# Optimization experiments

Measured on AMD Instinct MI355X. Metric: run time of the kernel, lower is better.

## Reference

```python
import jax, jax.numpy as jnp
import numpy as np

NUM_EMBEDDINGS = 1024
EMBEDDING_DIM = 64


def setup_inputs() -> dict:
    key = jax.random.key(0)
    kx, kc = jax.random.split(key)
    x = jax.random.normal(kx, (32, 64, 64, EMBEDDING_DIM), dtype=jnp.float32)
    # flax nn.Embed default init: normal(stddev=1.0)
    codebook = jax.random.normal(kc, (NUM_EMBEDDINGS, EMBEDDING_DIM), dtype=jnp.float32)
    return {"x": x, "codebook": codebook}


def reference(x, codebook):
    # x: [B, H, W, D] -> [N, D]
    x_flat = x.reshape(-1, EMBEDDING_DIM)
    distances = (
        jnp.sum(x_flat ** 2, axis=1, keepdims=True)
        - 2.0 * jnp.dot(x_flat, codebook.T)
        + jnp.sum(codebook ** 2, axis=1)
    )
    idx = jnp.argmin(distances, axis=1)                      # [N]
    discrete = jax.nn.one_hot(idx, NUM_EMBEDDINGS, dtype=x.dtype)  # [N, K]
    quantized = jnp.dot(discrete, codebook)                  # [N, D]
    quantized = quantized.reshape(x.shape[:-1] + (-1,))
    return (discrete, quantized)
```

## Files before the change

kernel.cpp:

```cpp
#include <hip/hip_runtime.h>

#define KCW 1024
#define DIM 64
#define ROWS_BLK 256
#define STRIPE 128
#define CWTILE 128

typedef __attribute__((ext_vector_type(4))) float f32x4;

__global__ void __launch_bounds__(256) vq_cnorm_kernel(const float* __restrict__ cb,
                                                       float* __restrict__ cnorm) {
    int k = blockIdx.x * blockDim.x + threadIdx.x;
    if (k < KCW) {
        const float4* c4 = (const float4*)(cb + (size_t)k * DIM);
        float s0 = 0.f, s1 = 0.f, s2 = 0.f, s3 = 0.f;
#pragma unroll
        for (int j = 0; j < DIM / 4; j += 4) {
            float4 a = c4[j + 0];
            float4 b = c4[j + 1];
            float4 c = c4[j + 2];
            float4 d = c4[j + 3];
            s0 += a.x * a.x + a.y * a.y + a.z * a.z + a.w * a.w;
            s1 += b.x * b.x + b.y * b.y + b.z * b.z + b.w * b.w;
            s2 += c.x * c.x + c.y * c.y + c.z * c.z + c.w * c.w;
            s3 += d.x * d.x + d.y * d.y + d.z * d.z + d.w * d.w;
        }
        cnorm[k] = (s0 + s1) + (s2 + s3);
    }
}

#define DOT4ACC(acc, av, bv)                                               \
    acc = fmaf((av).w, (bv).w,                                             \
          fmaf((av).z, (bv).z,                                             \
          fmaf((av).y, (bv).y,                                             \
          fmaf((av).x, (bv).x, (acc)))));

#define ROWF(P, n)                                                         \
    DOT4ACC(q##n##a.x, r##P##n, c##P##0) DOT4ACC(q##n##a.y, r##P##n, c##P##1) \
    DOT4ACC(q##n##a.z, r##P##n, c##P##2) DOT4ACC(q##n##a.w, r##P##n, c##P##3) \
    DOT4ACC(q##n##b.x, r##P##n, c##P##4) DOT4ACC(q##n##b.y, r##P##n, c##P##5) \
    DOT4ACC(q##n##b.z, r##P##n, c##P##6) DOT4ACC(q##n##b.w, r##P##n, c##P##7)

#define FMAB(P) ROWF(P, 0) ROWF(P, 1) ROWF(P, 2) ROWF(P, 3)                \
                ROWF(P, 4) ROWF(P, 5) ROWF(P, 6) ROWF(P, 7)

#define LOADOPS(P, k4v)                                                    \
    {   const int ka_ = (k4v) ^ ty2;                                       \
        const int kb_ = (k4v) ^ tx2;                                       \
        r##P##0 = sX[abase + ka_ + 0 * 128];                               \
        r##P##1 = sX[abase + ka_ + 1 * 128];                               \
        r##P##2 = sX[abase + ka_ + 2 * 128];                               \
        r##P##3 = sX[abase + ka_ + 3 * 128];                               \
        r##P##4 = sX[abase + ka_ + 4 * 128];                               \
        r##P##5 = sX[abase + ka_ + 5 * 128];                               \
        r##P##6 = sX[abase + ka_ + 6 * 128];                               \
        r##P##7 = sX[abase + ka_ + 7 * 128];                               \
        c##P##0 = sC[bbase + kb_ + 0 * 128];                               \
        c##P##1 = sC[bbase + kb_ + 1 * 128];                               \
        c##P##2 = sC[bbase + kb_ + 2 * 128];                               \
        c##P##3 = sC[bbase + kb_ + 3 * 128];                               \
        c##P##4 = sC[bbase + kb_ + 4 * 128];                               \
        c##P##5 = sC[bbase + kb_ + 5 * 128];                               \
        c##P##6 = sC[bbase + kb_ + 6 * 128];                               \
        c##P##7 = sC[bbase + kb_ + 7 * 128]; }

#define UPROW(n, X)                                                        \
    { float s_ = fmaf(-2.f, q##n##X, cn);                                  \
      if (s_ < best##n) { best##n = s_; bidx##n = cwv; } }

#define UPCOL(c, X)                                                        \
    { const float cn = sCn[cnb + 8 * (c)];                                 \
      const int cwv = cwbase + 8 * (c);                                    \
      UPROW(0, X) UPROW(1, X) UPROW(2, X) UPROW(3, X)                      \
      UPROW(4, X) UPROW(5, X) UPROW(6, X) UPROW(7, X) }

#define MERGEPUT(n)                                                        \
    { int rl = 64 * wr + ty + 8 * (n);                                     \
      sMs[rl * 16 + slot] = best##n; sMi[rl * 16 + slot] = bidx##n; }

__global__ void __launch_bounds__(256, 2) vq_main_kernel(const float* __restrict__ x,
                                                         const float* __restrict__ cb,
                                                         const float* __restrict__ cnorm,
                                                         float* __restrict__ out_discrete,
                                                         float* __restrict__ out_quant) {
    __shared__ float4 sX[STRIPE * 16];
    __shared__ float4 sC[CWTILE * 16];
    __shared__ float sCn[CWTILE];
    __shared__ int sFinal[STRIPE];

    float* sMs = (float*)sX;
    int* sMi = ((int*)sX) + STRIPE * 16;

    const int tid = threadIdx.x;
    const int wave = tid >> 6;
    const int lane = tid & 63;
    const int wr = wave >> 1;
    const int wc = wave & 1;
    const int ty = lane >> 3;
    const int tx = lane & 7;

    const int row0 = blockIdx.x * ROWS_BLK;
    const float4* xg = (const float4*)x;
    const float4* cbg = (const float4*)cb;
    float4* od4 = (float4*)out_discrete;
    float4* oq4 = (float4*)out_quant;

    const int cnb = 64 * wc + tx;
    const int abase = (64 * wr + ty) * 16;
    const int bbase = (64 * wc + tx) * 16;
    const int ty2 = ty << 1;
    const int tx2 = tx << 1;
    const int slot = wc * 8 + tx;

    for (int s = 0; s < ROWS_BLK / STRIPE; ++s) {
        const int grow0 = row0 + s * STRIPE;

        __syncthreads();

#pragma unroll
        for (int i = 0; i < 8; ++i) {
            int e = i * 256 + tid;
            int r = e >> 4, ch = e & 15;
            sX[r * 16 + (ch ^ ((r & 7) << 1))] = xg[(size_t)(grow0 + r) * 16 + ch];
        }

        float best0 = 3.4e38f, best1 = 3.4e38f, best2 = 3.4e38f, best3 = 3.4e38f;
        float best4 = 3.4e38f, best5 = 3.4e38f, best6 = 3.4e38f, best7 = 3.4e38f;
        int bidx0 = 0, bidx1 = 0, bidx2 = 0, bidx3 = 0;
        int bidx4 = 0, bidx5 = 0, bidx6 = 0, bidx7 = 0;

        for (int p = 0; p < KCW / CWTILE; ++p) {
            __syncthreads();

#pragma unroll
            for (int i = 0; i < 8; ++i) {
                int e = i * 256 + tid;
                int c = e >> 4, ch = e & 15;
                sC[c * 16 + (ch ^ ((c & 7) << 1))] =
                    cbg[(size_t)(p * CWTILE + c) * 16 + ch];
            }
            if (tid < CWTILE) sCn[tid] = cnorm[p * CWTILE + tid];
            __syncthreads();

            float4 q0a = {0.f, 0.f, 0.f, 0.f}, q0b = {0.f, 0.f, 0.f, 0.f};
            float4 q1a = {0.f, 0.f, 0.f, 0.f}, q1b = {0.f, 0.f, 0.f, 0.f};
            float4 q2a = {0.f, 0.f, 0.f, 0.f}, q2b = {0.f, 0.f, 0.f, 0.f};
            float4 q3a = {0.f, 0.f, 0.f, 0.f}, q3b = {0.f, 0.f, 0.f, 0.f};
            float4 q4a = {0.f, 0.f, 0.f, 0.f}, q4b = {0.f, 0.f, 0.f, 0.f};
            float4 q5a = {0.f, 0.f, 0.f, 0.f}, q5b = {0.f, 0.f, 0.f, 0.f};
            float4 q6a = {0.f, 0.f, 0.f, 0.f}, q6b = {0.f, 0.f, 0.f, 0.f};
            float4 q7a = {0.f, 0.f, 0.f, 0.f}, q7b = {0.f, 0.f, 0.f, 0.f};

            float4 rA0, rA1, rA2, rA3, rA4, rA5, rA6, rA7;
            float4 cA0, cA1, cA2, cA3, cA4, cA5, cA6, cA7;
            float4 rB0, rB1, rB2, rB3, rB4, rB5, rB6, rB7;
            float4 cB0, cB1, cB2, cB3, cB4, cB5, cB6, cB7;

            LOADOPS(A, 0)
#pragma unroll
            for (int k4 = 0; k4 < 16; k4 += 2) {
                LOADOPS(B, k4 + 1)
                FMAB(A)
                if (k4 + 2 < 16) LOADOPS(A, k4 + 2)
                FMAB(B)
            }

            const int cwbase = p * CWTILE + 64 * wc + tx;
            UPCOL(0, a.x) UPCOL(1, a.y) UPCOL(2, a.z) UPCOL(3, a.w)
            UPCOL(4, b.x) UPCOL(5, b.y) UPCOL(6, b.z) UPCOL(7, b.w)
        }

        __syncthreads();

        MERGEPUT(0) MERGEPUT(1) MERGEPUT(2) MERGEPUT(3)
        MERGEPUT(4) MERGEPUT(5) MERGEPUT(6) MERGEPUT(7)
        __syncthreads();

        if (tid < STRIPE) {
            float bs = sMs[tid * 16];
            int bi = sMi[tid * 16];
#pragma unroll
            for (int j = 1; j < 16; ++j) {
                float sj = sMs[tid * 16 + j];
                int ij = sMi[tid * 16 + j];
                if (sj < bs || (sj == bs && ij < bi)) { bs = sj; bi = ij; }
            }
            sFinal[tid] = bi;
        }
        __syncthreads();

        {
            size_t obase = (size_t)grow0 * (KCW / 4);
            const int col = tid * 4;
            for (int it = 0; it < STRIPE; ++it) {
                int idx = sFinal[it];
                f32x4 v;
                v.x = (col + 0 == idx) ? 1.f : 0.f;
                v.y = (col + 1 == idx) ? 1.f : 0.f;
                v.z = (col + 2 == idx) ? 1.f : 0.f;
                v.w = (col + 3 == idx) ? 1.f : 0.f;
                __builtin_nontemporal_store(v, (f32x4*)&od4[obase + (size_t)it * 256 + tid]);
            }
            size_t qbase = (size_t)grow0 * 16;
#pragma unroll
            for (int it = 0; it < 8; ++it) {
                int cnk = it * 256 + tid;
                int r = cnk >> 4;
                int ch = cnk & 15;
                float4 qv = cbg[(size_t)sFinal[r] * 16 + ch];
                __builtin_nontemporal_store(*(f32x4*)&qv, (f32x4*)&oq4[qbase + cnk]);
            }
        }
    }
}

extern "C" void kernel_launch(void* const* d_in, const int* in_sizes, int n_in,
                              void* d_out, int out_size, void* d_ws, size_t ws_size,
                              hipStream_t stream) {
    const float* x = (const float*)d_in[0];
    const float* cb = (const float*)d_in[1];
    float* cnorm = (float*)d_ws;

    const int n = in_sizes[0];
    const int rows = n / DIM;

    float* out_discrete = (float*)d_out;
    float* out_quant = (float*)d_out + (size_t)rows * KCW;

    vq_cnorm_kernel<<<(KCW + 255) / 256, 256, 0, stream>>>(cb, cnorm);
    vq_main_kernel<<<rows / ROWS_BLK, 256, 0, stream>>>(x, cb, cnorm, out_discrete, out_quant);
}
```

Before: 816.6 us.

## Keep X stripe rows in registers and split codeword tile into halves

Each thread now preloads its 8 input rows (all 64 dims) from shared memory into a register array once per stripe. The dot-product loop then reads only codebook vectors from shared memory, processing the 8 per-thread codewords in two halves of 4 to cut accumulator count. The aim is to remove the repeated LDS reads of X for every codebook tile. The cost is a 512-float register array per thread, which likely exceeds the VGPR budget under the two-blocks-per-CU launch bound and risks heavy scratch spilling.

```diff
diff --git a/kernel.cpp b/kernel.cpp
--- a/kernel.cpp
+++ b/kernel.cpp
@@ -35,44 +35,34 @@
           fmaf((av).y, (bv).y,                                             \
           fmaf((av).x, (bv).x, (acc)))));
 
-#define ROWF(P, n)                                                         \
-    DOT4ACC(q##n##a.x, r##P##n, c##P##0) DOT4ACC(q##n##a.y, r##P##n, c##P##1) \
-    DOT4ACC(q##n##a.z, r##P##n, c##P##2) DOT4ACC(q##n##a.w, r##P##n, c##P##3) \
-    DOT4ACC(q##n##b.x, r##P##n, c##P##4) DOT4ACC(q##n##b.y, r##P##n, c##P##5) \
-    DOT4ACC(q##n##b.z, r##P##n, c##P##6) DOT4ACC(q##n##b.w, r##P##n, c##P##7)
-
-#define FMAB(P) ROWF(P, 0) ROWF(P, 1) ROWF(P, 2) ROWF(P, 3)                \
-                ROWF(P, 4) ROWF(P, 5) ROWF(P, 6) ROWF(P, 7)
-
-#define LOADOPS(P, k4v)                                                    \
-    {   const int ka_ = (k4v) ^ ty2;                                       \
-        const int kb_ = (k4v) ^ tx2;                                       \
-        r##P##0 = sX[abase + ka_ + 0 * 128];                               \
-        r##P##1 = sX[abase + ka_ + 1 * 128];                               \
-        r##P##2 = sX[abase + ka_ + 2 * 128];                               \
-        r##P##3 = sX[abase + ka_ + 3 * 128];                               \
-        r##P##4 = sX[abase + ka_ + 4 * 128];                               \
-        r##P##5 = sX[abase + ka_ + 5 * 128];                               \
-        r##P##6 = sX[abase + ka_ + 6 * 128];                               \
-        r##P##7 = sX[abase + ka_ + 7 * 128];                               \
-        c##P##0 = sC[bbase + kb_ + 0 * 128];                               \
-        c##P##1 = sC[bbase + kb_ + 1 * 128];                               \
-        c##P##2 = sC[bbase + kb_ + 2 * 128];                               \
-        c##P##3 = sC[bbase + kb_ + 3 * 128];                               \
-        c##P##4 = sC[bbase + kb_ + 4 * 128];                               \
-        c##P##5 = sC[bbase + kb_ + 5 * 128];                               \
-        c##P##6 = sC[bbase + kb_ + 6 * 128];                               \
-        c##P##7 = sC[bbase + kb_ + 7 * 128]; }
-
-#define UPROW(n, X)                                                        \
-    { float s_ = fmaf(-2.f, q##n##X, cn);                                  \
-      if (s_ < best##n) { best##n = s_; bidx##n = cwv; } }
-
-#define UPCOL(c, X)                                                        \
-    { const float cn = sCn[cnb + 8 * (c)];                                 \
-      const int cwv = cwbase + 8 * (c);                                    \
-      UPROW(0, X) UPROW(1, X) UPROW(2, X) UPROW(3, X)                      \
-      UPROW(4, X) UPROW(5, X) UPROW(6, X) UPROW(7, X) }
+#define LOADQ(P, k4v, h)                                                   \
+    {   const int kb_ = ((k4v) ^ tx2);                                     \
+        P##0 = sC[bbase + kb_ + ((h) * 4 + 0) * 128];                      \
+        P##1 = sC[bbase + kb_ + ((h) * 4 + 1) * 128];                      \
+        P##2 = sC[bbase + kb_ + ((h) * 4 + 2) * 128];                      \
+        P##3 = sC[bbase + kb_ + ((h) * 4 + 3) * 128]; }
+
+#define ROWQ(P, n, k4v)                                                    \
+    DOT4ACC(q##n.x, areg[n][(k4v)], P##0)                                  \
+    DOT4ACC(q##n.y, areg[n][(k4v)], P##1)                                  \
+    DOT4ACC(q##n.z, areg[n][(k4v)], P##2)                                  \
+    DOT4ACC(q##n.w, areg[n][(k4v)], P##3)
+
+#define FMAQ(P, k4v) ROWQ(P, 0, (k4v)) ROWQ(P, 1, (k4v)) ROWQ(P, 2, (k4v)) \
+                     ROWQ(P, 3, (k4v)) ROWQ(P, 4, (k4v)) ROWQ(P, 5, (k4v)) \
+                     ROWQ(P, 6, (k4v)) ROWQ(P, 7, (k4v))
+
+#define UPR(n, comp)                                                       \
+    { float s_ = fmaf(-2.f, q##n.comp, cn_);                               \
+      if (s_ < best##n) { best##n = s_; bidx##n = cwv_; } }
+
+#define UPC(c, comp, h)                                                    \
+    { const float cn_ = sCn[cnb + 8 * (4 * (h) + (c))];                    \
+      const int cwv_ = cwbase + 8 * (4 * (h) + (c));                       \
+      UPR(0, comp) UPR(1, comp) UPR(2, comp) UPR(3, comp)                  \
+      UPR(4, comp) UPR(5, comp) UPR(6, comp) UPR(7, comp) }
+
+#define UPQUAD(h) UPC(0, x, (h)) UPC(1, y, (h)) UPC(2, z, (h)) UPC(3, w, (h))
 
 #define MERGEPUT(n)                                                        \
     { int rl = 64 * wr + ty + 8 * (n);                                     \
@@ -106,7 +96,6 @@
     float4* oq4 = (float4*)out_quant;
 
     const int cnb = 64 * wc + tx;
-    const int abase = (64 * wr + ty) * 16;
     const int bbase = (64 * wc + tx) * 16;
     const int ty2 = ty << 1;
     const int tx2 = tx << 1;
@@ -122,6 +111,16 @@
             int e = i * 256 + tid;
             int r = e >> 4, ch = e & 15;
             sX[r * 16 + (ch ^ ((r & 7) << 1))] = xg[(size_t)(grow0 + r) * 16 + ch];
+        }
+        __syncthreads();
+
+        float4 areg[8][16];
+#pragma unroll
+        for (int n = 0; n < 8; ++n) {
+            const int rb = (64 * wr + ty + 8 * n) * 16;
+#pragma unroll
+            for (int j = 0; j < 16; ++j)
+                areg[n][j] = sX[rb + (j ^ ty2)];
         }
 
         float best0 = 3.4e38f, best1 = 3.4e38f, best2 = 3.4e38f, best3 = 3.4e38f;
@@ -142,32 +141,29 @@
             if (tid < CWTILE) sCn[tid] = cnorm[p * CWTILE + tid];
             __syncthreads();
 
-            float4 q0a = {0.f, 0.f, 0.f, 0.f}, q0b = {0.f, 0.f, 0.f, 0.f};
-            float4 q1a = {0.f, 0.f, 0.f, 0.f}, q1b = {0.f, 0.f, 0.f, 0.f};
-            float4 q2a = {0.f, 0.f, 0.f, 0.f}, q2b = {0.f, 0.f, 0.f, 0.f};
-            float4 q3a = {0.f, 0.f, 0.f, 0.f}, q3b = {0.f, 0.f, 0.f, 0.f};
-            float4 q4a = {0.f, 0.f, 0.f, 0.f}, q4b = {0.f, 0.f, 0.f, 0.f};
-            float4 q5a = {0.f, 0.f, 0.f, 0.f}, q5b = {0.f, 0.f, 0.f, 0.f};
-            float4 q6a = {0.f, 0.f, 0.f, 0.f}, q6b = {0.f, 0.f, 0.f, 0.f};
-            float4 q7a = {0.f, 0.f, 0.f, 0.f}, q7b = {0.f, 0.f, 0.f, 0.f};
-
-            float4 rA0, rA1, rA2, rA3, rA4, rA5, rA6, rA7;
-            float4 cA0, cA1, cA2, cA3, cA4, cA5, cA6, cA7;
-            float4 rB0, rB1, rB2, rB3, rB4, rB5, rB6, rB7;
-            float4 cB0, cB1, cB2, cB3, cB4, cB5, cB6, cB7;
-
-            LOADOPS(A, 0)
-#pragma unroll
-            for (int k4 = 0; k4 < 16; k4 += 2) {
-                LOADOPS(B, k4 + 1)
-                FMAB(A)
-                if (k4 + 2 < 16) LOADOPS(A, k4 + 2)
-                FMAB(B)
-            }
-
             const int cwbase = p * CWTILE + 64 * wc + tx;
-            UPCOL(0, a.x) UPCOL(1, a.y) UPCOL(2, a.z) UPCOL(3, a.w)
-            UPCOL(4, b.x) UPCOL(5, b.y) UPCOL(6, b.z) UPCOL(7, b.w)
+
+#pragma unroll
+            for (int h = 0; h < 2; ++h) {
+                float4 q0 = {0.f, 0.f, 0.f, 0.f}, q1 = {0.f, 0.f, 0.f, 0.f};
+                float4 q2 = {0.f, 0.f, 0.f, 0.f}, q3 = {0.f, 0.f, 0.f, 0.f};
+                float4 q4 = {0.f, 0.f, 0.f, 0.f}, q5 = {0.f, 0.f, 0.f, 0.f};
+                float4 q6 = {0.f, 0.f, 0.f, 0.f}, q7 = {0.f, 0.f, 0.f, 0.f};
+
+                float4 u0, u1, u2, u3;
+                float4 v0, v1, v2, v3;
+
+                LOADQ(u, 0, h)
+#pragma unroll
+                for (int k4 = 0; k4 < 16; k4 += 2) {
+                    LOADQ(v, k4 + 1, h)
+                    FMAQ(u, k4)
+                    if (k4 + 2 < 16) LOADQ(u, k4 + 2, h)
+                    FMAQ(v, k4 + 1)
+                }
+
+                UPQUAD(h)
+            }
         }
 
         __syncthreads();
```

New measurement: 2.531 ms. 3.1x slower.
